# Performance work log

Hardware: AMD Instinct MI355X
Metric: run time of the kernel (lower is better)

## Reference

```python
import jax, jax.numpy as jnp
import numpy as np
import math

B, T, C = 4, 2048, 1024
NH = 16
HS = C // NH

def setup_inputs() -> dict:
    key = jax.random.key(0)
    ks = jax.random.split(key, 5)
    s = 0.02
    return {
        "x": jax.random.normal(ks[0], (B, T, C), dtype=jnp.float32),
        "W_attn": jax.random.normal(ks[1], (C, 3 * C), dtype=jnp.float32) * s,
        "b_attn": jax.random.normal(ks[2], (3 * C,), dtype=jnp.float32) * s,
        "W_proj": jax.random.normal(ks[3], (C, C), dtype=jnp.float32) * s,
        "b_proj": jax.random.normal(ks[4], (C,), dtype=jnp.float32) * s,
    }

def reference(x, W_attn, b_attn, W_proj, b_proj):
    Bx, Tx, Cx = x.shape
    qkv = x @ W_attn + b_attn                      # [B,T,3C]
    q, k, v = jnp.split(qkv, 3, axis=-1)
    # [B,T,C] -> [B,nh,T,hs]
    def heads(t):
        return t.reshape(Bx, Tx, NH, HS).transpose(0, 2, 1, 3)
    q, k, v = heads(q), heads(k), heads(v)
    att = jnp.einsum('bhqd,bhkd->bhqk', q, k) * (1.0 / math.sqrt(HS))
    causal = jnp.tril(jnp.ones((Tx, Tx), dtype=bool))
    att = jnp.where(causal[None, None], att, -jnp.inf)
    att = jax.nn.softmax(att, axis=-1)
    y = jnp.einsum('bhqk,bhkd->bhqd', att, v)      # [B,nh,T,hs]
    y = y.transpose(0, 2, 1, 3).reshape(Bx, Tx, Cx)
    return y @ W_proj + b_proj
```

## Files before the change

### kernel.cpp

```cpp
#include <hip/hip_runtime.h>
#include <hip/hip_bf16.h>
#include <stdint.h>

typedef __bf16 bf16x8 __attribute__((ext_vector_type(8)));
typedef __bf16 bf16x4 __attribute__((ext_vector_type(4)));
typedef float  f32x4  __attribute__((ext_vector_type(4)));

#define MFMA16(a, b, c) __builtin_amdgcn_mfma_f32_16x16x32_bf16((a), (b), (c), 0, 0, 0)

constexpr int BATCH = 4;
constexpr int TSEQ  = 2048;
constexpr int CDIM  = 1024;
constexpr int NHEAD = 16;
constexpr int HSZ   = 64;
constexpr size_t HEADELEMS = (size_t)BATCH * NHEAD * TSEQ * HSZ;

constexpr int LDF = 72;

__device__ __forceinline__ void load_lds_128(const __bf16* g, __bf16* l) {
    __builtin_amdgcn_global_load_lds(
        (const __attribute__((address_space(1))) unsigned int*)g,
        (__attribute__((address_space(3))) unsigned int*)l,
        16, 0, 0);
}

__global__ void conv_f32_bf16(const float* __restrict__ src, __bf16* __restrict__ dst, int n)
{
    const int i0 = (blockIdx.x * 256 + threadIdx.x) * 8;
    if (i0 >= n) return;
    float4 a = *(const float4*)(src + i0);
    float4 b = *(const float4*)(src + i0 + 4);
    bf16x8 o;
    o[0] = (__bf16)a.x; o[1] = (__bf16)a.y; o[2] = (__bf16)a.z; o[3] = (__bf16)a.w;
    o[4] = (__bf16)b.x; o[5] = (__bf16)b.y; o[6] = (__bf16)b.z; o[7] = (__bf16)b.w;
    *(bf16x8*)(dst + i0) = o;
}

__global__ void conv_transpose_bf16(const float* __restrict__ src, __bf16* __restrict__ dst,
                                    int K, int N)
{
    __shared__ __bf16 tile[32][33];
    const int n0 = blockIdx.x * 32, k0 = blockIdx.y * 32;
    const int tx = threadIdx.x & 31, ty = threadIdx.x >> 5;
    #pragma unroll
    for (int i = 0; i < 32; i += 8)
        tile[ty + i][tx] = (__bf16)src[(size_t)(k0 + ty + i) * N + n0 + tx];
    __syncthreads();
    #pragma unroll
    for (int i = 0; i < 32; i += 8)
        dst[(size_t)(n0 + ty + i) * K + k0 + tx] = tile[tx][ty + i];
}

template<int EPI>
__global__ __launch_bounds__(256, 4)
void gemm_bt(const __bf16* __restrict__ A, const __bf16* __restrict__ BT,
             const float* __restrict__ bias, void* __restrict__ outv,
             int M, int N, int K)
{
    __shared__ __bf16 As[2][128 * 32];
    __shared__ __bf16 Bs[2][128 * 32];

    const int t    = threadIdx.x;
    const int wave = t >> 6, lane = t & 63;
    const int quad = lane >> 4, l16 = lane & 15;
    const int bm = blockIdx.y * 128, bn = blockIdx.x * 128;
    const int wm = (wave >> 1) * 64, wn = (wave & 1) * 64;

    const int lrow = lane >> 2, lchunk = lane & 3;

    f32x4 acc[4][4];
    #pragma unroll
    for (int i = 0; i < 4; ++i)
        #pragma unroll
        for (int j = 0; j < 4; ++j)
            acc[i][j] = (f32x4){0.f, 0.f, 0.f, 0.f};

    const int c0 = wave * 2, c1 = wave * 2 + 1;
    const __bf16* a0 = A  + (size_t)(bm + 16 * c0 + lrow) * K + 8 * lchunk;
    const __bf16* a1 = A  + (size_t)(bm + 16 * c1 + lrow) * K + 8 * lchunk;
    const __bf16* b0 = BT + (size_t)(bn + 16 * c0 + lrow) * K + 8 * lchunk;
    const __bf16* b1 = BT + (size_t)(bn + 16 * c1 + lrow) * K + 8 * lchunk;

    const int nk = K >> 5;
    load_lds_128(a0, &As[0][c0 * 512]);
    load_lds_128(a1, &As[0][c1 * 512]);
    load_lds_128(b0, &Bs[0][c0 * 512]);
    load_lds_128(b1, &Bs[0][c1 * 512]);

    for (int it = 0; it < nk; ++it) {
        asm volatile("s_waitcnt vmcnt(0)" ::: "memory");
        __syncthreads();
        const int cur = it & 1, nxt = cur ^ 1;
        if (it + 1 < nk) {
            const int k0 = (it + 1) * 32;
            load_lds_128(a0 + k0, &As[nxt][c0 * 512]);
            load_lds_128(a1 + k0, &As[nxt][c1 * 512]);
            load_lds_128(b0 + k0, &Bs[nxt][c0 * 512]);
            load_lds_128(b1 + k0, &Bs[nxt][c1 * 512]);
        }

        bf16x8 af[4], bfr[4];
        #pragma unroll
        for (int i = 0; i < 4; ++i)
            af[i]  = *(const bf16x8*)(&As[cur][(wm + i * 16 + l16) * 32 + quad * 8]);
        #pragma unroll
        for (int i = 0; i < 4; ++i)
            bfr[i] = *(const bf16x8*)(&Bs[cur][(wn + i * 16 + l16) * 32 + quad * 8]);
        #pragma unroll
        for (int mi = 0; mi < 4; ++mi)
            #pragma unroll
            for (int ni = 0; ni < 4; ++ni)
                acc[mi][ni] = MFMA16(af[mi], bfr[ni], acc[mi][ni]);
    }

    if constexpr (EPI == 0) {
        __bf16* outp = (__bf16*)outv;
        #pragma unroll
        for (int ni = 0; ni < 4; ++ni) {
            const int col = bn + wn + ni * 16 + l16;
            const float bv = bias[col];
            const int which = col >> 10;
            const int c = col & 1023;
            const int h = c >> 6, d = c & 63;
            #pragma unroll
            for (int mi = 0; mi < 4; ++mi)
                #pragma unroll
                for (int r = 0; r < 4; ++r) {
                    const int row = bm + wm + mi * 16 + quad * 4 + r;
                    const int bb = row >> 11, tt = row & 2047;
                    size_t idx;
                    if (which == 2)
                        idx = 2 * HEADELEMS + ((((size_t)bb * NHEAD + h) * HSZ + d) * TSEQ + tt);
                    else
                        idx = (size_t)which * HEADELEMS
                            + ((((size_t)bb * NHEAD + h) * TSEQ + tt) * HSZ + d);
                    outp[idx] = (__bf16)(acc[mi][ni][r] + bv);
                }
        }
    } else {
        float* outp = (float*)outv;
        #pragma unroll
        for (int ni = 0; ni < 4; ++ni) {
            const int col = bn + wn + ni * 16 + l16;
            const float bv = bias[col];
            #pragma unroll
            for (int mi = 0; mi < 4; ++mi)
                #pragma unroll
                for (int r = 0; r < 4; ++r) {
                    const int row = bm + wm + mi * 16 + quad * 4 + r;
                    outp[(size_t)row * N + col] = acc[mi][ni][r] + bv;
                }
        }
    }
}

__global__ __launch_bounds__(256, 4)
void flash_attn(const __bf16* __restrict__ Q, const __bf16* __restrict__ Kg,
                const __bf16* __restrict__ Vg, __bf16* __restrict__ Y)
{
    __shared__ __bf16 Ks[64 * LDF];
    __shared__ __bf16 Vs[64 * LDF];
    __shared__ __bf16 Ps[4][32 * LDF];

    const int t = threadIdx.x, wave = t >> 6, lane = t & 63;
    const int quad = lane >> 4, l16 = lane & 15;
    const int bh = blockIdx.x;
    const int q0 = ((int)gridDim.y - 1 - (int)blockIdx.y) * 128;
    const size_t base = (size_t)bh * TSEQ * HSZ;

    const float sc = 0.125f * 1.44269504088896341f;

    bf16x8 qf[2][2];
    #pragma unroll
    for (int mi = 0; mi < 2; ++mi) {
        const int qrow = q0 + wave * 32 + mi * 16 + l16;
        #pragma unroll
        for (int h = 0; h < 2; ++h) {
            bf16x8 raw = *(const bf16x8*)(Q + base + (size_t)qrow * HSZ + h * 32 + quad * 8);
            #pragma unroll
            for (int j = 0; j < 8; ++j) qf[mi][h][j] = (__bf16)((float)raw[j] * sc);
        }
    }

    bf16x8 ones;
    #pragma unroll
    for (int j = 0; j < 8; ++j) ones[j] = (__bf16)1.0f;

    f32x4 oacc[2][4];
    f32x4 lacc[2];
    #pragma unroll
    for (int mi = 0; mi < 2; ++mi) {
        lacc[mi] = (f32x4){0.f, 0.f, 0.f, 0.f};
        #pragma unroll
        for (int dt = 0; dt < 4; ++dt) oacc[mi][dt] = (f32x4){0.f, 0.f, 0.f, 0.f};
    }

    const int s_row = t >> 2, s_c16 = (t & 3) * 16;

    const int iters = q0 / 64 + 2;
    for (int it = 0; it < iters; ++it) {
        const int kt = it * 64;
        {
            const __bf16* kp = Kg + base + (size_t)(kt + s_row) * HSZ + s_c16;
            bf16x8 v0 = *(const bf16x8*)kp;
            bf16x8 v1 = *(const bf16x8*)(kp + 8);
            *(bf16x8*)(&Ks[s_row * LDF + s_c16])     = v0;
            *(bf16x8*)(&Ks[s_row * LDF + s_c16 + 8]) = v1;
        }
        {
            const __bf16* vp = Vg + base + (size_t)s_row * TSEQ + kt + s_c16;
            bf16x8 v0 = *(const bf16x8*)vp;
            bf16x8 v1 = *(const bf16x8*)(vp + 8);
            *(bf16x8*)(&Vs[s_row * LDF + s_c16])     = v0;
            *(bf16x8*)(&Vs[s_row * LDF + s_c16 + 8]) = v1;
        }
        __syncthreads();

        const bool active = (kt <= q0 + wave * 32 + 31);
        if (active) {
            f32x4 st[4][2];
            #pragma unroll
            for (int ktl = 0; ktl < 4; ++ktl) {
                bf16x8 kf0 = *(const bf16x8*)(&Ks[(ktl * 16 + l16) * LDF + quad * 8]);
                bf16x8 kf1 = *(const bf16x8*)(&Ks[(ktl * 16 + l16) * LDF + 32 + quad * 8]);
                #pragma unroll
                for (int mi = 0; mi < 2; ++mi) {
                    f32x4 a = (f32x4){0.f, 0.f, 0.f, 0.f};
                    a = MFMA16(kf0, qf[mi][0], a);
                    a = MFMA16(kf1, qf[mi][1], a);
                    st[ktl][mi] = a;
                }
            }

            if (kt + 63 >= q0 + wave * 32) {
                #pragma unroll
                for (int ktl = 0; ktl < 4; ++ktl)
                    #pragma unroll
                    for (int mi = 0; mi < 2; ++mi)
                        #pragma unroll
                        for (int r = 0; r < 4; ++r) {
                            const int key = kt + ktl * 16 + quad * 4 + r;
                            const int qr  = q0 + wave * 32 + mi * 16 + l16;
                            if (key > qr) st[ktl][mi][r] = -1e30f;
                        }
            }

            #pragma unroll
            for (int ktl = 0; ktl < 4; ++ktl)
                #pragma unroll
                for (int mi = 0; mi < 2; ++mi) {
                    bf16x4 pv;
                    #pragma unroll
                    for (int r = 0; r < 4; ++r)
                        pv[r] = (__bf16)exp2f(st[ktl][mi][r]);
                    *(bf16x4*)(&Ps[wave][(mi * 16 + l16) * LDF + ktl * 16 + quad * 4]) = pv;
                }

            asm volatile("s_waitcnt lgkmcnt(0)" ::: "memory");

            bf16x8 pf[2][2];
            #pragma unroll
            for (int mi = 0; mi < 2; ++mi) {
                pf[mi][0] = *(const bf16x8*)(&Ps[wave][(mi * 16 + l16) * LDF + quad * 8]);
                pf[mi][1] = *(const bf16x8*)(&Ps[wave][(mi * 16 + l16) * LDF + 32 + quad * 8]);
                lacc[mi] = MFMA16(pf[mi][0], ones, lacc[mi]);
                lacc[mi] = MFMA16(pf[mi][1], ones, lacc[mi]);
            }
            #pragma unroll
            for (int dt = 0; dt < 4; ++dt) {
                bf16x8 vf0 = *(const bf16x8*)(&Vs[(dt * 16 + l16) * LDF + quad * 8]);
                bf16x8 vf1 = *(const bf16x8*)(&Vs[(dt * 16 + l16) * LDF + 32 + quad * 8]);
                #pragma unroll
                for (int mi = 0; mi < 2; ++mi) {
                    oacc[mi][dt] = MFMA16(pf[mi][0], vf0, oacc[mi][dt]);
                    oacc[mi][dt] = MFMA16(pf[mi][1], vf1, oacc[mi][dt]);
                }
            }
        }
        __syncthreads();
    }

    const int b = bh >> 4, h = bh & 15;
    #pragma unroll
    for (int mi = 0; mi < 2; ++mi) {
        const f32x4 linv = {1.f / lacc[mi][0], 1.f / lacc[mi][1],
                            1.f / lacc[mi][2], 1.f / lacc[mi][3]};
        #pragma unroll
        for (int dt = 0; dt < 4; ++dt)
            #pragma unroll
            for (int r = 0; r < 4; ++r) {
                const int tt = q0 + wave * 32 + mi * 16 + quad * 4 + r;
                const int d  = dt * 16 + l16;
                Y[((size_t)(b * TSEQ + tt) * CDIM) + h * HSZ + d] =
                    (__bf16)(oacc[mi][dt][r] * linv[r]);
            }
    }
}

extern "C" void kernel_launch(void* const* d_in, const int* in_sizes, int n_in,
                              void* d_out, int out_size, void* d_ws, size_t ws_size,
                              hipStream_t stream)
{
    const int NX = 8388608, NWA = 3145728, NWP = 1048576;
    char* wsb = (char*)d_ws;

    size_t off = 0;
    __bf16* cx   = (__bf16*)(wsb + off); off += (size_t)2 * NX;
    __bf16* cwaT = (__bf16*)(wsb + off); off += (size_t)2 * NWA;
    __bf16* cwpT = (__bf16*)(wsb + off); off += (size_t)2 * NWP;
    __bf16* q    = (__bf16*)(wsb + off);
    __bf16* y    = q + 3 * HEADELEMS;

    const float* xf = (const float*)d_in[0];
    const float* ba = (const float*)d_in[2];
    const float* bp = (const float*)d_in[4];

    conv_f32_bf16<<<NX / 2048, 256, 0, stream>>>(xf, cx, NX);
    conv_transpose_bf16<<<dim3(3 * CDIM / 32, CDIM / 32), 256, 0, stream>>>(
        (const float*)d_in[1], cwaT, CDIM, 3 * CDIM);
    conv_transpose_bf16<<<dim3(CDIM / 32, CDIM / 32), 256, 0, stream>>>(
        (const float*)d_in[3], cwpT, CDIM, CDIM);

    gemm_bt<0><<<dim3(3 * CDIM / 128, BATCH * TSEQ / 128), 256, 0, stream>>>(
        cx, cwaT, ba, q, BATCH * TSEQ, 3 * CDIM, CDIM);

    flash_attn<<<dim3(BATCH * NHEAD, TSEQ / 128), 256, 0, stream>>>(
        q, q + HEADELEMS, q + 2 * HEADELEMS, y);

    gemm_bt<1><<<dim3(CDIM / 128, BATCH * TSEQ / 128), 256, 0, stream>>>(
        y, cwpT, bp, d_out, BATCH * TSEQ, CDIM, CDIM);
}
```

Measured before the change: 271.4 us.

## Triple-buffer GEMM loads and shrink flash-attention blocks to 64 query rows

The GEMM now keeps three LDS stages and prefetches two K-steps ahead, using a partial vmcnt wait instead of draining all loads each iteration, so global-to-LDS latency overlaps more with MFMA work. This raises LDS use per block and lowers the occupancy target to 3 blocks. Flash attention switches to 128-thread blocks covering 64 query rows, which doubles the grid, cuts wasted masked work on the causal diagonal, and removes the per-wave active check. In exchange, each K/V tile loaded into LDS serves fewer query rows.

Result: slower. 290.0 us (+6.9%).

```diff
diff --git a/kernel.cpp b/kernel.cpp
--- a/kernel.cpp
+++ b/kernel.cpp
@@ -52,13 +52,13 @@
 }
 
 template<int EPI>
-__global__ __launch_bounds__(256, 4)
-void gemm_bt(const __bf16* __restrict__ A, const __bf16* __restrict__ BT,
-             const float* __restrict__ bias, void* __restrict__ outv,
-             int M, int N, int K)
-{
-    __shared__ __bf16 As[2][128 * 32];
-    __shared__ __bf16 Bs[2][128 * 32];
+__global__ __launch_bounds__(256, 3)
+void gemm_bt_pipe(const __bf16* __restrict__ A, const __bf16* __restrict__ BT,
+                  const float* __restrict__ bias, void* __restrict__ outv,
+                  int M, int N, int K)
+{
+    __shared__ __bf16 As[3][128 * 32];
+    __shared__ __bf16 Bs[3][128 * 32];
 
     const int t    = threadIdx.x;
     const int wave = t >> 6, lane = t & 63;
@@ -82,21 +82,26 @@
     const __bf16* b1 = BT + (size_t)(bn + 16 * c1 + lrow) * K + 8 * lchunk;
 
     const int nk = K >> 5;
-    load_lds_128(a0, &As[0][c0 * 512]);
-    load_lds_128(a1, &As[0][c1 * 512]);
-    load_lds_128(b0, &Bs[0][c0 * 512]);
-    load_lds_128(b1, &Bs[0][c1 * 512]);
-
+
+#define STAGE(buf, kofs) do { \
+    load_lds_128(a0 + (kofs), &As[buf][c0 * 512]); \
+    load_lds_128(a1 + (kofs), &As[buf][c1 * 512]); \
+    load_lds_128(b0 + (kofs), &Bs[buf][c0 * 512]); \
+    load_lds_128(b1 + (kofs), &Bs[buf][c1 * 512]); } while (0)
+
+    STAGE(0, 0);
+    if (nk > 1) STAGE(1, 32);
+
+    int cur = 0;
     for (int it = 0; it < nk; ++it) {
-        asm volatile("s_waitcnt vmcnt(0)" ::: "memory");
-        __syncthreads();
-        const int cur = it & 1, nxt = cur ^ 1;
-        if (it + 1 < nk) {
-            const int k0 = (it + 1) * 32;
-            load_lds_128(a0 + k0, &As[nxt][c0 * 512]);
-            load_lds_128(a1 + k0, &As[nxt][c1 * 512]);
-            load_lds_128(b0 + k0, &Bs[nxt][c0 * 512]);
-            load_lds_128(b1 + k0, &Bs[nxt][c1 * 512]);
+        if (it + 1 < nk) asm volatile("s_waitcnt vmcnt(4)" ::: "memory");
+        else             asm volatile("s_waitcnt vmcnt(0)" ::: "memory");
+        __builtin_amdgcn_s_barrier();
+        __builtin_amdgcn_sched_barrier(0);
+
+        if (it + 2 < nk) {
+            const int stg = (cur >= 1) ? cur - 1 : cur + 2;
+            STAGE(stg, (it + 2) * 32);
         }
 
         bf16x8 af[4], bfr[4];
@@ -111,7 +116,10 @@
             #pragma unroll
             for (int ni = 0; ni < 4; ++ni)
                 acc[mi][ni] = MFMA16(af[mi], bfr[ni], acc[mi][ni]);
-    }
+
+        cur = (cur + 1 >= 3) ? 0 : cur + 1;
+    }
+#undef STAGE
 
     if constexpr (EPI == 0) {
         __bf16* outp = (__bf16*)outv;
@@ -154,18 +162,18 @@
     }
 }
 
-__global__ __launch_bounds__(256, 4)
+__global__ __launch_bounds__(128, 4)
 void flash_attn(const __bf16* __restrict__ Q, const __bf16* __restrict__ Kg,
                 const __bf16* __restrict__ Vg, __bf16* __restrict__ Y)
 {
     __shared__ __bf16 Ks[64 * LDF];
     __shared__ __bf16 Vs[64 * LDF];
-    __shared__ __bf16 Ps[4][32 * LDF];
+    __shared__ __bf16 Ps[2][32 * LDF];
 
     const int t = threadIdx.x, wave = t >> 6, lane = t & 63;
     const int quad = lane >> 4, l16 = lane & 15;
     const int bh = blockIdx.x;
-    const int q0 = ((int)gridDim.y - 1 - (int)blockIdx.y) * 128;
+    const int q0 = ((int)gridDim.y - 1 - (int)blockIdx.y) * 64;
     const size_t base = (size_t)bh * TSEQ * HSZ;
 
     const float sc = 0.125f * 1.44269504088896341f;
@@ -197,27 +205,36 @@
 
     const int s_row = t >> 2, s_c16 = (t & 3) * 16;
 
-    const int iters = q0 / 64 + 2;
+    const int iters = q0 / 64 + 1;
     for (int it = 0; it < iters; ++it) {
         const int kt = it * 64;
         {
-            const __bf16* kp = Kg + base + (size_t)(kt + s_row) * HSZ + s_c16;
-            bf16x8 v0 = *(const bf16x8*)kp;
-            bf16x8 v1 = *(const bf16x8*)(kp + 8);
-            *(bf16x8*)(&Ks[s_row * LDF + s_c16])     = v0;
-            *(bf16x8*)(&Ks[s_row * LDF + s_c16 + 8]) = v1;
+            const __bf16* kp0 = Kg + base + (size_t)(kt + s_row) * HSZ + s_c16;
+            const __bf16* kp1 = kp0 + (size_t)32 * HSZ;
+            bf16x8 v0 = *(const bf16x8*)kp0;
+            bf16x8 v1 = *(const bf16x8*)(kp0 + 8);
+            bf16x8 v2 = *(const bf16x8*)kp1;
+            bf16x8 v3 = *(const bf16x8*)(kp1 + 8);
+            *(bf16x8*)(&Ks[s_row * LDF + s_c16])            = v0;
+            *(bf16x8*)(&Ks[s_row * LDF + s_c16 + 8])        = v1;
+            *(bf16x8*)(&Ks[(s_row + 32) * LDF + s_c16])     = v2;
+            *(bf16x8*)(&Ks[(s_row + 32) * LDF + s_c16 + 8]) = v3;
         }
         {
-            const __bf16* vp = Vg + base + (size_t)s_row * TSEQ + kt + s_c16;
-            bf16x8 v0 = *(const bf16x8*)vp;
-            bf16x8 v1 = *(const bf16x8*)(vp + 8);
-            *(bf16x8*)(&Vs[s_row * LDF + s_c16])     = v0;
-            *(bf16x8*)(&Vs[s_row * LDF + s_c16 + 8]) = v1;
+            const __bf16* vp0 = Vg + base + (size_t)s_row * TSEQ + kt + s_c16;
+            const __bf16* vp1 = vp0 + (size_t)32 * TSEQ;
+            bf16x8 v0 = *(const bf16x8*)vp0;
+            bf16x8 v1 = *(const bf16x8*)(vp0 + 8);
+            bf16x8 v2 = *(const bf16x8*)vp1;
+            bf16x8 v3 = *(const bf16x8*)(vp1 + 8);
+            *(bf16x8*)(&Vs[s_row * LDF + s_c16])            = v0;
+            *(bf16x8*)(&Vs[s_row * LDF + s_c16 + 8])        = v1;
+            *(bf16x8*)(&Vs[(s_row + 32) * LDF + s_c16])     = v2;
+            *(bf16x8*)(&Vs[(s_row + 32) * LDF + s_c16 + 8]) = v3;
         }
         __syncthreads();
 
-        const bool active = (kt <= q0 + wave * 32 + 31);
-        if (active) {
+        {
             f32x4 st[4][2];
             #pragma unroll
             for (int ktl = 0; ktl < 4; ++ktl) {
@@ -321,12 +338,12 @@
     conv_transpose_bf16<<<dim3(CDIM / 32, CDIM / 32), 256, 0, stream>>>(
         (const float*)d_in[3], cwpT, CDIM, CDIM);
 
-    gemm_bt<0><<<dim3(3 * CDIM / 128, BATCH * TSEQ / 128), 256, 0, stream>>>(
+    gemm_bt_pipe<0><<<dim3(3 * CDIM / 128, BATCH * TSEQ / 128), 256, 0, stream>>>(
         cx, cwaT, ba, q, BATCH * TSEQ, 3 * CDIM, CDIM);
 
-    flash_attn<<<dim3(BATCH * NHEAD, TSEQ / 128), 256, 0, stream>>>(
+    flash_attn<<<dim3(BATCH * NHEAD, TSEQ / 64), 128, 0, stream>>>(
         q, q + HEADELEMS, q + 2 * HEADELEMS, y);
 
-    gemm_bt<1><<<dim3(CDIM / 128, BATCH * TSEQ / 128), 256, 0, stream>>>(
+    gemm_bt_pipe<1><<<dim3(CDIM / 128, BATCH * TSEQ / 128), 256, 0, stream>>>(
         y, cwpT, bp, d_out, BATCH * TSEQ, CDIM, CDIM);
 }
```

## Triple-buffer GEMM K-loop, swizzle block order, fuse prep conversion kernels

Applied to the files above, without the earlier changes.

The GEMM moves from double to triple-buffered LDS staging with a partial vmcnt wait, so each iteration overlaps two pending tile loads instead of draining all of them. Block indices are remapped in strides of 8 to group tiles, likely to spread them across the chip's XCDs for L2 locality. The three fp32-to-bf16 conversion and transpose launches are merged into one kernel to cut launch overhead. The extra buffer raises LDS use and lowers launch_bounds occupancy from 4 to 3 blocks.

After: 262.7 us. -3.2%, faster.

```diff
diff --git a/kernel.cpp b/kernel.cpp
--- a/kernel.cpp
+++ b/kernel.cpp
@@ -24,23 +24,30 @@
         16, 0, 0);
 }
 
-__global__ void conv_f32_bf16(const float* __restrict__ src, __bf16* __restrict__ dst, int n)
-{
-    const int i0 = (blockIdx.x * 256 + threadIdx.x) * 8;
-    if (i0 >= n) return;
-    float4 a = *(const float4*)(src + i0);
-    float4 b = *(const float4*)(src + i0 + 4);
-    bf16x8 o;
-    o[0] = (__bf16)a.x; o[1] = (__bf16)a.y; o[2] = (__bf16)a.z; o[3] = (__bf16)a.w;
-    o[4] = (__bf16)b.x; o[5] = (__bf16)b.y; o[6] = (__bf16)b.z; o[7] = (__bf16)b.w;
-    *(bf16x8*)(dst + i0) = o;
-}
-
-__global__ void conv_transpose_bf16(const float* __restrict__ src, __bf16* __restrict__ dst,
-                                    int K, int N)
+__global__ __launch_bounds__(256)
+void prep_fused(const float* __restrict__ x, __bf16* __restrict__ cx,
+                const float* __restrict__ wa, __bf16* __restrict__ cwaT,
+                const float* __restrict__ wp, __bf16* __restrict__ cwpT)
 {
     __shared__ __bf16 tile[32][33];
-    const int n0 = blockIdx.x * 32, k0 = blockIdx.y * 32;
+    const int blk = blockIdx.x;
+
+    if (blk < 4096) {
+        const int i0 = (blk * 256 + (int)threadIdx.x) * 8;
+        float4 a = *(const float4*)(x + i0);
+        float4 b = *(const float4*)(x + i0 + 4);
+        bf16x8 o;
+        o[0] = (__bf16)a.x; o[1] = (__bf16)a.y; o[2] = (__bf16)a.z; o[3] = (__bf16)a.w;
+        o[4] = (__bf16)b.x; o[5] = (__bf16)b.y; o[6] = (__bf16)b.z; o[7] = (__bf16)b.w;
+        *(bf16x8*)(cx + i0) = o;
+        return;
+    }
+
+    const float* src;  __bf16* dst;  int K, N, bidx;
+    if (blk < 7168) { src = wa; dst = cwaT; K = 1024; N = 3072; bidx = blk - 4096; }
+    else            { src = wp; dst = cwpT; K = 1024; N = 1024; bidx = blk - 7168; }
+    const int nbx = N >> 5;
+    const int n0 = (bidx % nbx) * 32, k0 = (bidx / nbx) * 32;
     const int tx = threadIdx.x & 31, ty = threadIdx.x >> 5;
     #pragma unroll
     for (int i = 0; i < 32; i += 8)
@@ -52,18 +59,25 @@
 }
 
 template<int EPI>
-__global__ __launch_bounds__(256, 4)
-void gemm_bt(const __bf16* __restrict__ A, const __bf16* __restrict__ BT,
-             const float* __restrict__ bias, void* __restrict__ outv,
-             int M, int N, int K)
+__global__ __launch_bounds__(256, 3)
+void gemm_bt_pipe(const __bf16* __restrict__ A, const __bf16* __restrict__ BT,
+                  const float* __restrict__ bias, void* __restrict__ outv,
+                  int M, int N, int K)
 {
-    __shared__ __bf16 As[2][128 * 32];
-    __shared__ __bf16 Bs[2][128 * 32];
+    __shared__ __bf16 As[3][128 * 32];
+    __shared__ __bf16 Bs[3][128 * 32];
 
     const int t    = threadIdx.x;
     const int wave = t >> 6, lane = t & 63;
     const int quad = lane >> 4, l16 = lane & 15;
-    const int bm = blockIdx.y * 128, bn = blockIdx.x * 128;
+
+    const int nbx = (int)gridDim.x;
+    int lin = (int)blockIdx.y * nbx + (int)blockIdx.x;
+    {
+        const int cpx = (nbx * (int)gridDim.y) >> 3;
+        lin = (lin & 7) * cpx + (lin >> 3);
+    }
+    const int bm = (lin / nbx) * 128, bn = (lin % nbx) * 128;
     const int wm = (wave >> 1) * 64, wn = (wave & 1) * 64;
 
     const int lrow = lane >> 2, lchunk = lane & 3;
@@ -82,21 +96,26 @@
     const __bf16* b1 = BT + (size_t)(bn + 16 * c1 + lrow) * K + 8 * lchunk;
 
     const int nk = K >> 5;
-    load_lds_128(a0, &As[0][c0 * 512]);
-    load_lds_128(a1, &As[0][c1 * 512]);
-    load_lds_128(b0, &Bs[0][c0 * 512]);
-    load_lds_128(b1, &Bs[0][c1 * 512]);
-
+
+#define STAGE(buf, kofs) do { \
+    load_lds_128(a0 + (kofs), &As[buf][c0 * 512]); \
+    load_lds_128(a1 + (kofs), &As[buf][c1 * 512]); \
+    load_lds_128(b0 + (kofs), &Bs[buf][c0 * 512]); \
+    load_lds_128(b1 + (kofs), &Bs[buf][c1 * 512]); } while (0)
+
+    STAGE(0, 0);
+    if (nk > 1) STAGE(1, 32);
+
+    int cur = 0;
     for (int it = 0; it < nk; ++it) {
-        asm volatile("s_waitcnt vmcnt(0)" ::: "memory");
-        __syncthreads();
-        const int cur = it & 1, nxt = cur ^ 1;
-        if (it + 1 < nk) {
-            const int k0 = (it + 1) * 32;
-            load_lds_128(a0 + k0, &As[nxt][c0 * 512]);
-            load_lds_128(a1 + k0, &As[nxt][c1 * 512]);
-            load_lds_128(b0 + k0, &Bs[nxt][c0 * 512]);
-            load_lds_128(b1 + k0, &Bs[nxt][c1 * 512]);
+        if (it + 1 < nk) asm volatile("s_waitcnt vmcnt(4)" ::: "memory");
+        else             asm volatile("s_waitcnt vmcnt(0)" ::: "memory");
+        __builtin_amdgcn_s_barrier();
+        __builtin_amdgcn_sched_barrier(0);
+
+        if (it + 2 < nk) {
+            const int stg = (cur >= 1) ? cur - 1 : cur + 2;
+            STAGE(stg, (it + 2) * 32);
         }
 
         bf16x8 af[4], bfr[4];
@@ -111,7 +130,10 @@
             #pragma unroll
             for (int ni = 0; ni < 4; ++ni)
                 acc[mi][ni] = MFMA16(af[mi], bfr[ni], acc[mi][ni]);
-    }
+
+        cur = (cur + 1 >= 3) ? 0 : cur + 1;
+    }
+#undef STAGE
 
     if constexpr (EPI == 0) {
         __bf16* outp = (__bf16*)outv;
@@ -315,18 +337,15 @@
     const float* ba = (const float*)d_in[2];
     const float* bp = (const float*)d_in[4];
 
-    conv_f32_bf16<<<NX / 2048, 256, 0, stream>>>(xf, cx, NX);
-    conv_transpose_bf16<<<dim3(3 * CDIM / 32, CDIM / 32), 256, 0, stream>>>(
-        (const float*)d_in[1], cwaT, CDIM, 3 * CDIM);
-    conv_transpose_bf16<<<dim3(CDIM / 32, CDIM / 32), 256, 0, stream>>>(
-        (const float*)d_in[3], cwpT, CDIM, CDIM);
-
-    gemm_bt<0><<<dim3(3 * CDIM / 128, BATCH * TSEQ / 128), 256, 0, stream>>>(
+    prep_fused<<<8192, 256, 0, stream>>>(
+        xf, cx, (const float*)d_in[1], cwaT, (const float*)d_in[3], cwpT);
+
+    gemm_bt_pipe<0><<<dim3(3 * CDIM / 128, BATCH * TSEQ / 128), 256, 0, stream>>>(
         cx, cwaT, ba, q, BATCH * TSEQ, 3 * CDIM, CDIM);
 
     flash_attn<<<dim3(BATCH * NHEAD, TSEQ / 128), 256, 0, stream>>>(
         q, q + HEADELEMS, q + 2 * HEADELEMS, y);
 
-    gemm_bt<1><<<dim3(CDIM / 128, BATCH * TSEQ / 128), 256, 0, stream>>>(
+    gemm_bt_pipe<1><<<dim3(CDIM / 128, BATCH * TSEQ / 128), 256, 0, stream>>>(
         y, cwpT, bp, d_out, BATCH * TSEQ, CDIM, CDIM);
 }
```
